# Optimization experiments

Measured on AMD Instinct MI355X. Metric: run time of the kernel, lower is better.

The kernel has to match this reference:

```python
import jax, jax.numpy as jnp
import numpy as np
from jax import lax

NUM_CLASSES = 9
N_BOXES = 6
LEVELS = [(32, 256), (16, 128), (8, 64), (4, 32), (2, 16), (1, 8)]
BATCH = 8


def _conv(x, w, b):
    # x: [N,C,H,W], w: [O,I,3,3] -> same-padded stride-1 conv (padding=1)
    y = lax.conv_general_dilated(x, w, window_strides=(1, 1), padding='SAME',
                                 dimension_numbers=('NCHW', 'OIHW', 'NCHW'))
    return y + b[None, :, None, None]


def _head(x, ws, bs, w_out, b_out):
    for i in range(4):
        x = jax.nn.relu(_conv(x, ws[i], bs[i]))
    return _conv(x, w_out, b_out)


def setup_inputs() -> dict:
    key = jax.random.key(0)
    ks = jax.random.split(key, 12)
    inp = {}
    for i, (h, w) in enumerate(LEVELS):
        inp[f'feat{i}'] = jax.random.normal(ks[i], (BATCH, 256, h, w), dtype=jnp.float32)
    std = 0.01  # matches _init_improved_weights: normal(0, 0.01), bias=0
    inp['reg_w'] = jax.random.normal(ks[6], (4, 256, 256, 3, 3), dtype=jnp.float32) * std
    inp['reg_b'] = jnp.zeros((4, 256), dtype=jnp.float32)
    inp['reg_w_out'] = jax.random.normal(ks[7], (N_BOXES * 4, 256, 3, 3), dtype=jnp.float32) * std
    inp['reg_b_out'] = jnp.zeros((N_BOXES * 4,), dtype=jnp.float32)
    inp['cls_w'] = jax.random.normal(ks[8], (4, 256, 256, 3, 3), dtype=jnp.float32) * std
    inp['cls_b'] = jnp.zeros((4, 256), dtype=jnp.float32)
    inp['cls_w_out'] = jax.random.normal(ks[9], (N_BOXES * NUM_CLASSES, 256, 3, 3), dtype=jnp.float32) * std
    inp['cls_b_out'] = jnp.zeros((N_BOXES * NUM_CLASSES,), dtype=jnp.float32)
    return inp


def reference(feat0, feat1, feat2, feat3, feat4, feat5,
              reg_w, reg_b, reg_w_out, reg_b_out,
              cls_w, cls_b, cls_w_out, cls_b_out):
    features = [feat0, feat1, feat2, feat3, feat4, feat5]
    locations, confidences = [], []
    for x in features:
        n = x.shape[0]
        bbox_delta = _head(x, reg_w, reg_b, reg_w_out, reg_b_out).reshape(n, 4, -1)
        bbox_conf = _head(x, cls_w, cls_b, cls_w_out, cls_b_out).reshape(n, NUM_CLASSES, -1)
        locations.append(bbox_delta)
        confidences.append(bbox_conf)
    bbox_delta = jnp.concatenate(locations, axis=2)   # [N, 4, total_anchors]
    confs = jnp.concatenate(confidences, axis=2)      # [N, num_classes, total_anchors]
    return (bbox_delta, confs)
```

## Files before the change

### kernel.cpp

```cpp
#include <hip/hip_runtime.h>
#include <hip/hip_bf16.h>


typedef float  f32x4 __attribute__((ext_vector_type(4)));
typedef int    i32x4 __attribute__((ext_vector_type(4)));
typedef __bf16 bfrag __attribute__((ext_vector_type(8)));
typedef __bf16 bf4   __attribute__((ext_vector_type(4)));

struct LevelD {
  int H, W, logW, logHW, P, HW, act_off, aoff, blk_start, pos_start;
};
struct Desc  { LevelD lv[6]; };
struct FPtrs { const float* f[6]; };

#define ACT_ELEMS  24735744
#define WREG_OFF   0
#define WCLS_OFF   2359296
#define WREGO_OFF  4718592
#define WCLSO_OFF  4773888
#define ACT0_OFF   4898304
#define ACT1_OFF   29634048
#define WS_ELEMS   54369792ull
#define TOTAL_ANCH 65520
#define CLS_BASE   2096640

__device__ __forceinline__ void glds16(const __bf16* g, __bf16* l) {
  __builtin_amdgcn_global_load_lds(
      (const __attribute__((address_space(1))) void*)g,
      (__attribute__((address_space(3))) void*)l, 16, 0, 0);
}

__device__ __forceinline__ int xcd_swz(int b, int nwg) {
  int xcd = b & 7;
  int q = nwg >> 3, r = nwg & 7;
  int base = (xcd < r) ? xcd * (q + 1) : r * (q + 1) + (xcd - r) * q;
  return base + (b >> 3);
}

__global__ __launch_bounds__(256) void prep_k(const float* __restrict__ w,
                                              __bf16* __restrict__ o, int total)
{
  for (int i = blockIdx.x * 256 + threadIdx.x; i < total; i += gridDim.x * 256) {
    int co = i / 2304;
    int r  = i - co * 2304;
    int t  = r >> 8;
    int ci = r & 255;
    o[i] = (__bf16)w[((co << 8) + ci) * 9 + t];
  }
}

__global__ __launch_bounds__(256) void convert_k(FPtrs fp, __bf16* __restrict__ act, Desc d)
{
  __shared__ __bf16 T[16 * 264];
  int b  = blockIdx.x;
  int p0 = b << 4;
  int li = 0;
  #pragma unroll
  for (int i = 1; i < 6; ++i) li = (p0 >= d.lv[i].pos_start) ? i : li;
  LevelD L = d.lv[li];
  int lp  = b * 16 - L.pos_start;
  int tid = threadIdx.x;
  int pl = tid & 15;
  int p  = lp + pl;
  int n  = p >> L.logHW;
  int y  = (p >> L.logW) & (L.H - 1);
  int x  = p & (L.W - 1);
  const float* src = fp.f[li];
  size_t base = (size_t)n * ((size_t)L.HW << 8) + (size_t)y * L.W + x;
  int c0 = tid >> 4;
  #pragma unroll
  for (int it = 0; it < 16; ++it) {
    int c = c0 + (it << 4);
    T[pl * 264 + c] = (__bf16)src[base + (size_t)c * L.HW];
  }
  __syncthreads();
  int p2 = tid >> 4;
  int cc = (tid & 15) << 4;
  int pg = lp + p2;
  int n2 = pg >> L.logHW;
  int y2 = (pg >> L.logW) & (L.H - 1);
  int x2 = pg & (L.W - 1);
  __bf16* dst = act + L.act_off +
      ((size_t)((n2 * (L.H + 2) + y2 + 1) * (L.W + 2) + x2 + 1) << 8) + cc;
  i32x4 v0 = *(const i32x4*)&T[p2 * 264 + cc];
  i32x4 v1 = *(const i32x4*)&T[p2 * 264 + cc + 8];
  *(i32x4*)dst       = v0;
  *(i32x4*)(dst + 8) = v1;
}

__global__ __launch_bounds__(256, 3)
void conv_mid_k(const __bf16* __restrict__ inb, __bf16* __restrict__ outb,
                const __bf16* __restrict__ wT, const float* __restrict__ bias,
                Desc d)
{
  __shared__ __bf16 Al[2][128 * 32];
  __shared__ __bf16 Bl[2][128 * 32];
  int b  = xcd_swz(blockIdx.x, 1366);
  int li = 0;
  #pragma unroll
  for (int i = 1; i < 6; ++i) li = (b >= d.lv[i].blk_start) ? i : li;
  LevelD L  = d.lv[li];
  int local = b - L.blk_start;
  int mt = local & 1;
  int nt = local >> 1;
  int m0 = mt << 7;
  int p0 = nt << 7;
  int tid  = threadIdx.x;
  int lane = tid & 63;
  int wv   = tid >> 6;
  int wm = wv >> 1, wn = wv & 1;
  int fr = lane & 15, fg = lane >> 4;
  int Wp = L.W + 2;

  int rsub = lane >> 2;
  int slot = lane & 3;
  int sw   = slot ^ ((rsub >> 1) & 3);

  const __bf16* gA[2];
  const __bf16* gB[2];
  int ldsA[2];
  #pragma unroll
  for (int r = 0; r < 2; ++r) {
    int row = (r << 6) + (wv << 4) + rsub;
    gA[r] = wT + (m0 + row) * 2304 + (sw << 3);
    int p  = p0 + row;
    int pc = (p < L.P) ? p : 0;
    int n  = pc >> L.logHW;
    int y  = (pc >> L.logW) & (L.H - 1);
    int x  = pc & (L.W - 1);
    gB[r] = inb + L.act_off + (((n * (L.H + 2) + y) * Wp + x) << 8) + (sw << 3);
    ldsA[r] = ((r << 6) + (wv << 4)) << 5;
  }

  int csw = ((fg ^ ((fr >> 1) & 3)) << 3);
  int offA[4], offB[4];
  #pragma unroll
  for (int f = 0; f < 4; ++f) {
    offA[f] = (((wm << 6) + (f << 4) + fr) << 5) + csw;
    offB[f] = (((wn << 6) + (f << 4) + fr) << 5) + csw;
  }

  auto stage = [&](int k, int bb) {
    int t  = k >> 3;
    int c0 = (k & 7) << 5;
    int ky = (t >= 6) ? 2 : (t >= 3 ? 1 : 0);
    int kx = t - ky * 3;
    int koffA = (t << 8) + c0;
    int koffB = ((ky * Wp + kx) << 8) + c0;
    glds16(gA[0] + koffA, &Al[bb][ldsA[0]]);
    glds16(gA[1] + koffA, &Al[bb][ldsA[1]]);
    glds16(gB[0] + koffB, &Bl[bb][ldsA[0]]);
    glds16(gB[1] + koffB, &Bl[bb][ldsA[1]]);
  };

  f32x4 acc[4][4] = {};

  stage(0, 0);
  #pragma unroll 1
  for (int k = 0; k < 72; ++k) {
    int cur = k & 1;
    __syncthreads();
    if (k < 71) stage(k + 1, cur ^ 1);
    bfrag af[4], bfv[4];
    #pragma unroll
    for (int mf = 0; mf < 4; ++mf) af[mf]  = *(const bfrag*)&Al[cur][offA[mf]];
    #pragma unroll
    for (int nf = 0; nf < 4; ++nf) bfv[nf] = *(const bfrag*)&Bl[cur][offB[nf]];
    #pragma unroll
    for (int mf = 0; mf < 4; ++mf)
      #pragma unroll
      for (int nf = 0; nf < 4; ++nf)
        acc[mf][nf] = __builtin_amdgcn_mfma_f32_16x16x32_bf16(af[mf], bfv[nf],
                                                              acc[mf][nf], 0, 0, 0);
  }

  #pragma unroll
  for (int nf = 0; nf < 4; ++nf) {
    int pp = p0 + (wn << 6) + (nf << 4) + fr;
    if (pp >= L.P) continue;
    int n2 = pp >> L.logHW;
    int y2 = (pp >> L.logW) & (L.H - 1);
    int x2 = pp & (L.W - 1);
    __bf16* ob = outb + L.act_off + (((n2 * (L.H + 2) + y2 + 1) * Wp + x2 + 1) << 8);
    #pragma unroll
    for (int mf = 0; mf < 4; ++mf) {
      int cob = m0 + (wm << 6) + (mf << 4) + (fg << 2);
      f32x4 bb = *(const f32x4*)(bias + cob);
      f32x4 v  = acc[mf][nf];
      bf4 ov;
      #pragma unroll
      for (int j = 0; j < 4; ++j) ov[j] = (__bf16)fmaxf(v[j] + bb[j], 0.0f);
      *(bf4*)(ob + cob) = ov;
    }
  }
}

__global__ __launch_bounds__(256, 3)
void conv_out_k(const __bf16* __restrict__ inb, const __bf16* __restrict__ wT,
                const float* __restrict__ biasO, float* __restrict__ dout,
                Desc d, int Cout, int isCls)
{
  __shared__ __bf16 Asm[2][64 * 32];
  __shared__ __bf16 Bsm[2][128 * 32];
  int b  = xcd_swz(blockIdx.x, 683);
  int li = 0;
  #pragma unroll
  for (int i = 1; i < 6; ++i) li = (b >= d.lv[i].blk_start) ? i : li;
  LevelD L = d.lv[li];
  int p0 = (b - L.blk_start) << 7;
  int tid  = threadIdx.x;
  int lane = tid & 63;
  int wv   = tid >> 6;
  int fr = lane & 15, fg = lane >> 4;
  int Wp = L.W + 2;
  int nmf = (Cout + 15) >> 4;

  int rsub = lane >> 2;
  int slot = lane & 3;
  int sw   = slot ^ ((rsub >> 1) & 3);

  const __bf16* gA0;
  {
    int row = (wv << 4) + rsub;
    int co  = (row < Cout) ? row : 0;
    gA0 = wT + co * 2304 + (sw << 3);
  }
  const __bf16* gB[2];
  #pragma unroll
  for (int j = 0; j < 2; ++j) {
    int row = (j << 6) + (wv << 4) + rsub;
    int p  = p0 + row;
    int pc = (p < L.P) ? p : 0;
    int n = pc >> L.logHW, y = (pc >> L.logW) & (L.H - 1), x = pc & (L.W - 1);
    gB[j] = inb + L.act_off + (((n * (L.H + 2) + y) * Wp + x) << 8) + (sw << 3);
  }
  int dW = (wv << 4) << 5;

  int csw = ((fg ^ ((fr >> 1) & 3)) << 3);
  int offA[4], offB[2];
  #pragma unroll
  for (int mf = 0; mf < 4; ++mf)
    offA[mf] = (((mf << 4) + fr) << 5) + csw;
  #pragma unroll
  for (int nf = 0; nf < 2; ++nf)
    offB[nf] = (((wv << 5) + (nf << 4) + fr) << 5) + csw;

  auto stage = [&](int k, int bb) {
    int t  = k >> 3;
    int ky = (t >= 6) ? 2 : (t >= 3 ? 1 : 0);
    int kx = t - ky * 3;
    int ka = k << 5;
    int kb = ((ky * Wp + kx) << 8) + ((k & 7) << 5);
    glds16(gA0 + ka, &Asm[bb][dW]);
    glds16(gB[0] + kb, &Bsm[bb][dW]);
    glds16(gB[1] + kb, &Bsm[bb][2048 + dW]);
  };

  f32x4 acc[4][2] = {};

  stage(0, 0);
  #pragma unroll 1
  for (int k = 0; k < 72; ++k) {
    int cur = k & 1;
    __syncthreads();
    if (k < 71) stage(k + 1, cur ^ 1);
    bfrag af[4], bfv[2];
    #pragma unroll
    for (int mf = 0; mf < 4; ++mf)
      if (mf < nmf) af[mf] = *(const bfrag*)&Asm[cur][offA[mf]];
    #pragma unroll
    for (int nf = 0; nf < 2; ++nf)
      bfv[nf] = *(const bfrag*)&Bsm[cur][offB[nf]];
    #pragma unroll
    for (int mf = 0; mf < 4; ++mf)
      if (mf < nmf)
        #pragma unroll
        for (int nf = 0; nf < 2; ++nf)
          acc[mf][nf] = __builtin_amdgcn_mfma_f32_16x16x32_bf16(
              af[mf], bfv[nf], acc[mf][nf], 0, 0, 0);
  }

  #pragma unroll
  for (int nf = 0; nf < 2; ++nf) {
    int pp = p0 + (wv << 5) + (nf << 4) + fr;
    if (pp >= L.P) continue;
    int n2 = pp >> L.logHW;
    int y2 = (pp >> L.logW) & (L.H - 1);
    int x2 = pp & (L.W - 1);
    int sp_off = L.aoff + y2 * L.W + x2;
    #pragma unroll
    for (int mf = 0; mf < 4; ++mf) {
      if (mf < nmf) {
        #pragma unroll
        for (int j = 0; j < 4; ++j) {
          int co = (mf << 4) + (fg << 2) + j;
          if (co < Cout) {
            float val = acc[mf][nf][j] + biasO[co];
            int g   = co / 6;
            int box = co - g * 6;
            size_t idx;
            if (isCls) idx = (size_t)CLS_BASE + ((size_t)n2 * 9 + g) * TOTAL_ANCH
                             + sp_off + box * L.HW;
            else       idx = ((size_t)n2 * 4 + g) * TOTAL_ANCH + sp_off + box * L.HW;
            dout[idx] = val;
          }
        }
      }
    }
  }
}

extern "C" void kernel_launch(void* const* d_in, const int* in_sizes, int n_in,
                              void* d_out, int out_size, void* d_ws, size_t ws_size,
                              hipStream_t stream) {
  if (ws_size < WS_ELEMS * 2) return;

  static const int kH[6]      = {32, 16, 8, 4, 2, 1};
  static const int kW[6]      = {256, 128, 64, 32, 16, 8};
  static const int kLogW[6]   = {8, 7, 6, 5, 4, 3};
  static const int kLogHW[6]  = {13, 11, 9, 7, 5, 3};
  static const int kActOff[6] = {0, 17965056, 22757376, 24109056, 24526848, 24674304};
  static const int kAoff[6]   = {0, 49152, 61440, 64512, 65280, 65472};
  static const int kBlkMid[6] = {0, 1024, 1280, 1344, 1360, 1364};
  static const int kBlkOut[6] = {0, 512, 640, 672, 680, 682};
  static const int kPosSt[6]  = {0, 65536, 81920, 86016, 87040, 87296};

  FPtrs fp;
  for (int i = 0; i < 6; ++i) fp.f[i] = (const float*)d_in[i];
  const float* reg_w  = (const float*)d_in[6];
  const float* reg_b  = (const float*)d_in[7];
  const float* reg_wo = (const float*)d_in[8];
  const float* reg_bo = (const float*)d_in[9];
  const float* cls_w  = (const float*)d_in[10];
  const float* cls_b  = (const float*)d_in[11];
  const float* cls_wo = (const float*)d_in[12];
  const float* cls_bo = (const float*)d_in[13];
  __bf16* ws = (__bf16*)d_ws;

  Desc dmid, dout_d;
  for (int i = 0; i < 6; ++i) {
    LevelD L;
    L.H = kH[i]; L.W = kW[i]; L.logW = kLogW[i]; L.logHW = kLogHW[i];
    L.HW = kH[i] * kW[i]; L.P = 8 * L.HW;
    L.act_off = kActOff[i]; L.aoff = kAoff[i];
    L.pos_start = kPosSt[i];
    L.blk_start = kBlkMid[i];
    dmid.lv[i] = L;
    L.blk_start = kBlkOut[i];
    dout_d.lv[i] = L;
  }

  hipMemsetAsync((char*)d_ws + (size_t)ACT0_OFF * 2, 0,
                 (size_t)ACT_ELEMS * 2 * 2, stream);

  prep_k<<<256, 256, 0, stream>>>(reg_w,  ws + WREG_OFF,  1024 * 2304);
  prep_k<<<256, 256, 0, stream>>>(cls_w,  ws + WCLS_OFF,  1024 * 2304);
  prep_k<<<64,  256, 0, stream>>>(reg_wo, ws + WREGO_OFF, 24 * 2304);
  prep_k<<<64,  256, 0, stream>>>(cls_wo, ws + WCLSO_OFF, 54 * 2304);

  for (int head = 0; head < 2; ++head) {
    convert_k<<<5460, 256, 0, stream>>>(fp, ws + ACT0_OFF, dmid);
    const __bf16* wT = ws + (head ? WCLS_OFF : WREG_OFF);
    const float*  bb = head ? cls_b : reg_b;
    conv_mid_k<<<1366, 256, 0, stream>>>(ws + ACT0_OFF, ws + ACT1_OFF, wT + 0 * 589824, bb + 0,   dmid);
    conv_mid_k<<<1366, 256, 0, stream>>>(ws + ACT1_OFF, ws + ACT0_OFF, wT + 1 * 589824, bb + 256, dmid);
    conv_mid_k<<<1366, 256, 0, stream>>>(ws + ACT0_OFF, ws + ACT1_OFF, wT + 2 * 589824, bb + 512, dmid);
    conv_mid_k<<<1366, 256, 0, stream>>>(ws + ACT1_OFF, ws + ACT0_OFF, wT + 3 * 589824, bb + 768, dmid);
    conv_out_k<<<683, 256, 0, stream>>>(ws + ACT0_OFF,
        ws + (head ? WCLSO_OFF : WREGO_OFF), head ? cls_bo : reg_bo,
        (float*)d_out, dout_d, head ? 54 : 24, head);
  }
}
```

Measured before the change: 1.317 ms.

## Restructure mid conv into 8-wave 256x128 tile with triple-buffered staged pipeline

Replaces the 128x128, 4-wave, double-buffered implicit-GEMM conv kernel with a 512-thread kernel. Each block computes all 256 output channels for 128 positions, staging K=64 chunks through a 3-deep LDS ring. Global-to-LDS loads are interleaved between MFMA groups using explicit vmcnt waits, barriers, sched_barrier and setprio. This halves the grid, so each activation tile is loaded once instead of twice, and it aims to hide load latency behind matrix ops. The cost is one block per CU, larger LDS use, and more barriers per iteration.

```diff
diff --git a/kernel.cpp b/kernel.cpp
--- a/kernel.cpp
+++ b/kernel.cpp
@@ -88,23 +88,19 @@
   *(i32x4*)(dst + 8) = v1;
 }
 
-__global__ __launch_bounds__(256, 3)
-void conv_mid_k(const __bf16* __restrict__ inb, __bf16* __restrict__ outb,
-                const __bf16* __restrict__ wT, const float* __restrict__ bias,
-                Desc d)
+__global__ __launch_bounds__(512, 1)
+void conv_mid8_k(const __bf16* __restrict__ inb, __bf16* __restrict__ outb,
+                 const __bf16* __restrict__ wT, const float* __restrict__ bias,
+                 Desc d)
 {
-  __shared__ __bf16 Al[2][128 * 32];
-  __shared__ __bf16 Bl[2][128 * 32];
-  int b  = xcd_swz(blockIdx.x, 1366);
+  __shared__ __bf16 Asm[3 * 16384];
+  __shared__ __bf16 Bsm[3 * 8192];
+  int b  = xcd_swz(blockIdx.x, 683);
   int li = 0;
   #pragma unroll
   for (int i = 1; i < 6; ++i) li = (b >= d.lv[i].blk_start) ? i : li;
-  LevelD L  = d.lv[li];
-  int local = b - L.blk_start;
-  int mt = local & 1;
-  int nt = local >> 1;
-  int m0 = mt << 7;
-  int p0 = nt << 7;
+  LevelD L = d.lv[li];
+  int p0 = (b - L.blk_start) << 7;
   int tid  = threadIdx.x;
   int lane = tid & 63;
   int wv   = tid >> 6;
@@ -112,66 +108,135 @@
   int fr = lane & 15, fg = lane >> 4;
   int Wp = L.W + 2;
 
-  int rsub = lane >> 2;
-  int slot = lane & 3;
-  int sw   = slot ^ ((rsub >> 1) & 3);
-
-  const __bf16* gA[2];
+  int lrow8 = lane >> 3;
+  int lslot = lane & 7;
+  int wvb   = wv << 9;
+
+  const __bf16* gA[4];
+  #pragma unroll
+  for (int r = 0; r < 4; ++r) {
+    int row = (r << 6) + (wv << 3) + lrow8;
+    gA[r] = wT + row * 2304 + ((lslot ^ (row & 7)) << 3);
+  }
   const __bf16* gB[2];
-  int ldsA[2];
   #pragma unroll
   for (int r = 0; r < 2; ++r) {
-    int row = (r << 6) + (wv << 4) + rsub;
-    gA[r] = wT + (m0 + row) * 2304 + (sw << 3);
+    int row = (r << 6) + (wv << 3) + lrow8;
     int p  = p0 + row;
     int pc = (p < L.P) ? p : 0;
-    int n  = pc >> L.logHW;
-    int y  = (pc >> L.logW) & (L.H - 1);
-    int x  = pc & (L.W - 1);
-    gB[r] = inb + L.act_off + (((n * (L.H + 2) + y) * Wp + x) << 8) + (sw << 3);
-    ldsA[r] = ((r << 6) + (wv << 4)) << 5;
-  }
-
-  int csw = ((fg ^ ((fr >> 1) & 3)) << 3);
-  int offA[4], offB[4];
-  #pragma unroll
-  for (int f = 0; f < 4; ++f) {
-    offA[f] = (((wm << 6) + (f << 4) + fr) << 5) + csw;
-    offB[f] = (((wn << 6) + (f << 4) + fr) << 5) + csw;
-  }
-
-  auto stage = [&](int k, int bb) {
-    int t  = k >> 3;
-    int c0 = (k & 7) << 5;
-    int ky = (t >= 6) ? 2 : (t >= 3 ? 1 : 0);
-    int kx = t - ky * 3;
-    int koffA = (t << 8) + c0;
-    int koffB = ((ky * Wp + kx) << 8) + c0;
-    glds16(gA[0] + koffA, &Al[bb][ldsA[0]]);
-    glds16(gA[1] + koffA, &Al[bb][ldsA[1]]);
-    glds16(gB[0] + koffB, &Bl[bb][ldsA[0]]);
-    glds16(gB[1] + koffB, &Bl[bb][ldsA[1]]);
+    int n = pc >> L.logHW, y = (pc >> L.logW) & (L.H - 1), x = pc & (L.W - 1);
+    gB[r] = inb + L.act_off + (((n * (L.H + 2) + y) * Wp + x) << 8)
+            + ((lslot ^ (row & 7)) << 3);
+  }
+
+  int offA[4][2], offB[4][2];
+  #pragma unroll
+  for (int mf = 0; mf < 4; ++mf) {
+    int row = (wm << 6) + (mf << 4) + fr;
+    #pragma unroll
+    for (int kk = 0; kk < 2; ++kk)
+      offA[mf][kk] = (row << 6) + ((((kk << 2) | fg) ^ (row & 7)) << 3);
+  }
+  #pragma unroll
+  for (int nf = 0; nf < 4; ++nf) {
+    int row = (wn << 6) + (nf << 4) + fr;
+    #pragma unroll
+    for (int kk = 0; kk < 2; ++kk)
+      offB[nf][kk] = (row << 6) + ((((kk << 2) | fg) ^ (row & 7)) << 3);
+  }
+
+  auto stageA2 = [&](int k2, int buf, int r0) {
+    int ka = k2 << 6;
+    __bf16* dst = Asm + buf * 16384 + (r0 << 12) + wvb;
+    glds16(gA[r0] + ka, dst);
+    glds16(gA[r0 + 1] + ka, dst + 4096);
   };
+  auto stageB1 = [&](int k2, int buf, int r) {
+    int t2 = k2 >> 2;
+    int ky = (t2 >= 6) ? 2 : (t2 >= 3 ? 1 : 0);
+    int kx = t2 - ky * 3;
+    int kb = ((ky * Wp + kx) << 8) + ((k2 & 3) << 6);
+    glds16(gB[r] + kb, Bsm + buf * 8192 + (r << 12) + wvb);
+  };
 
   f32x4 acc[4][4] = {};
 
-  stage(0, 0);
+  stageA2(0, 0, 0); stageA2(0, 0, 2); stageB1(0, 0, 0); stageB1(0, 0, 1);
+  stageA2(1, 1, 0); stageA2(1, 1, 2); stageB1(1, 1, 0); stageB1(1, 1, 1);
+
+  int cur = 0;
   #pragma unroll 1
-  for (int k = 0; k < 72; ++k) {
-    int cur = k & 1;
-    __syncthreads();
-    if (k < 71) stage(k + 1, cur ^ 1);
-    bfrag af[4], bfv[4];
-    #pragma unroll
-    for (int mf = 0; mf < 4; ++mf) af[mf]  = *(const bfrag*)&Al[cur][offA[mf]];
-    #pragma unroll
-    for (int nf = 0; nf < 4; ++nf) bfv[nf] = *(const bfrag*)&Bl[cur][offB[nf]];
-    #pragma unroll
-    for (int mf = 0; mf < 4; ++mf)
-      #pragma unroll
-      for (int nf = 0; nf < 4; ++nf)
-        acc[mf][nf] = __builtin_amdgcn_mfma_f32_16x16x32_bf16(af[mf], bfv[nf],
-                                                              acc[mf][nf], 0, 0, 0);
+  for (int kt = 0; kt < 36; ++kt) {
+    int s2c = cur + 2; if (s2c >= 3) s2c -= 3;
+    int k2  = kt + 2;
+    bool st = (kt < 34);
+    const __bf16* Ab = Asm + cur * 16384;
+    const __bf16* Bb = Bsm + cur * 8192;
+
+    if (kt == 35) { asm volatile("s_waitcnt vmcnt(0)" ::: "memory"); }
+    else          { asm volatile("s_waitcnt vmcnt(6)" ::: "memory"); }
+    __builtin_amdgcn_s_barrier();
+    asm volatile("" ::: "memory");
+
+    bfrag bfv[4], af0, af1;
+    #pragma unroll
+    for (int nf = 0; nf < 4; ++nf) bfv[nf] = *(const bfrag*)&Bb[offB[nf][0]];
+    af0 = *(const bfrag*)&Ab[offA[0][0]];
+    af1 = *(const bfrag*)&Ab[offA[1][0]];
+    if (st) stageA2(k2, s2c, 0);
+    __builtin_amdgcn_s_barrier();
+    asm volatile("s_waitcnt lgkmcnt(0)" ::: "memory");
+    __builtin_amdgcn_sched_barrier(0);
+    __builtin_amdgcn_s_setprio(1);
+    #pragma unroll
+    for (int nf = 0; nf < 4; ++nf) {
+      acc[0][nf] = __builtin_amdgcn_mfma_f32_16x16x32_bf16(af0, bfv[nf], acc[0][nf], 0, 0, 0);
+      acc[1][nf] = __builtin_amdgcn_mfma_f32_16x16x32_bf16(af1, bfv[nf], acc[1][nf], 0, 0, 0);
+    }
+    __builtin_amdgcn_s_setprio(0);
+    af0 = *(const bfrag*)&Ab[offA[2][0]];
+    af1 = *(const bfrag*)&Ab[offA[3][0]];
+    if (st) stageA2(k2, s2c, 2);
+    __builtin_amdgcn_s_barrier();
+    asm volatile("s_waitcnt lgkmcnt(0)" ::: "memory");
+    __builtin_amdgcn_sched_barrier(0);
+    __builtin_amdgcn_s_setprio(1);
+    #pragma unroll
+    for (int nf = 0; nf < 4; ++nf) {
+      acc[2][nf] = __builtin_amdgcn_mfma_f32_16x16x32_bf16(af0, bfv[nf], acc[2][nf], 0, 0, 0);
+      acc[3][nf] = __builtin_amdgcn_mfma_f32_16x16x32_bf16(af1, bfv[nf], acc[3][nf], 0, 0, 0);
+    }
+    __builtin_amdgcn_s_setprio(0);
+    #pragma unroll
+    for (int nf = 0; nf < 4; ++nf) bfv[nf] = *(const bfrag*)&Bb[offB[nf][1]];
+    af0 = *(const bfrag*)&Ab[offA[0][1]];
+    af1 = *(const bfrag*)&Ab[offA[1][1]];
+    if (st) stageB1(k2, s2c, 0);
+    __builtin_amdgcn_s_barrier();
+    asm volatile("s_waitcnt lgkmcnt(0)" ::: "memory");
+    __builtin_amdgcn_sched_barrier(0);
+    __builtin_amdgcn_s_setprio(1);
+    #pragma unroll
+    for (int nf = 0; nf < 4; ++nf) {
+      acc[0][nf] = __builtin_amdgcn_mfma_f32_16x16x32_bf16(af0, bfv[nf], acc[0][nf], 0, 0, 0);
+      acc[1][nf] = __builtin_amdgcn_mfma_f32_16x16x32_bf16(af1, bfv[nf], acc[1][nf], 0, 0, 0);
+    }
+    __builtin_amdgcn_s_setprio(0);
+    af0 = *(const bfrag*)&Ab[offA[2][1]];
+    af1 = *(const bfrag*)&Ab[offA[3][1]];
+    if (st) stageB1(k2, s2c, 1);
+    __builtin_amdgcn_s_barrier();
+    asm volatile("s_waitcnt lgkmcnt(0)" ::: "memory");
+    __builtin_amdgcn_sched_barrier(0);
+    __builtin_amdgcn_s_setprio(1);
+    #pragma unroll
+    for (int nf = 0; nf < 4; ++nf) {
+      acc[2][nf] = __builtin_amdgcn_mfma_f32_16x16x32_bf16(af0, bfv[nf], acc[2][nf], 0, 0, 0);
+      acc[3][nf] = __builtin_amdgcn_mfma_f32_16x16x32_bf16(af1, bfv[nf], acc[3][nf], 0, 0, 0);
+    }
+    __builtin_amdgcn_s_setprio(0);
+
+    ++cur; if (cur == 3) cur = 0;
   }
 
   #pragma unroll
@@ -184,7 +249,7 @@
     __bf16* ob = outb + L.act_off + (((n2 * (L.H + 2) + y2 + 1) * Wp + x2 + 1) << 8);
     #pragma unroll
     for (int mf = 0; mf < 4; ++mf) {
-      int cob = m0 + (wm << 6) + (mf << 4) + (fg << 2);
+      int cob = (wm << 6) + (mf << 4) + (fg << 2);
       f32x4 bb = *(const f32x4*)(bias + cob);
       f32x4 v  = acc[mf][nf];
       bf4 ov;
@@ -321,8 +386,7 @@
   static const int kLogHW[6]  = {13, 11, 9, 7, 5, 3};
   static const int kActOff[6] = {0, 17965056, 22757376, 24109056, 24526848, 24674304};
   static const int kAoff[6]   = {0, 49152, 61440, 64512, 65280, 65472};
-  static const int kBlkMid[6] = {0, 1024, 1280, 1344, 1360, 1364};
-  static const int kBlkOut[6] = {0, 512, 640, 672, 680, 682};
+  static const int kBlk[6]    = {0, 512, 640, 672, 680, 682};
   static const int kPosSt[6]  = {0, 65536, 81920, 86016, 87040, 87296};
 
   FPtrs fp;
@@ -337,17 +401,14 @@
   const float* cls_bo = (const float*)d_in[13];
   __bf16* ws = (__bf16*)d_ws;
 
-  Desc dmid, dout_d;
+  Desc dd;
   for (int i = 0; i < 6; ++i) {
     LevelD L;
     L.H = kH[i]; L.W = kW[i]; L.logW = kLogW[i]; L.logHW = kLogHW[i];
     L.HW = kH[i] * kW[i]; L.P = 8 * L.HW;
     L.act_off = kActOff[i]; L.aoff = kAoff[i];
-    L.pos_start = kPosSt[i];
-    L.blk_start = kBlkMid[i];
-    dmid.lv[i] = L;
-    L.blk_start = kBlkOut[i];
-    dout_d.lv[i] = L;
+    L.blk_start = kBlk[i]; L.pos_start = kPosSt[i];
+    dd.lv[i] = L;
   }
 
   hipMemsetAsync((char*)d_ws + (size_t)ACT0_OFF * 2, 0,
@@ -359,15 +420,15 @@
   prep_k<<<64,  256, 0, stream>>>(cls_wo, ws + WCLSO_OFF, 54 * 2304);
 
   for (int head = 0; head < 2; ++head) {
-    convert_k<<<5460, 256, 0, stream>>>(fp, ws + ACT0_OFF, dmid);
+    convert_k<<<5460, 256, 0, stream>>>(fp, ws + ACT0_OFF, dd);
     const __bf16* wT = ws + (head ? WCLS_OFF : WREG_OFF);
     const float*  bb = head ? cls_b : reg_b;
-    conv_mid_k<<<1366, 256, 0, stream>>>(ws + ACT0_OFF, ws + ACT1_OFF, wT + 0 * 589824, bb + 0,   dmid);
-    conv_mid_k<<<1366, 256, 0, stream>>>(ws + ACT1_OFF, ws + ACT0_OFF, wT + 1 * 589824, bb + 256, dmid);
-    conv_mid_k<<<1366, 256, 0, stream>>>(ws + ACT0_OFF, ws + ACT1_OFF, wT + 2 * 589824, bb + 512, dmid);
-    conv_mid_k<<<1366, 256, 0, stream>>>(ws + ACT1_OFF, ws + ACT0_OFF, wT + 3 * 589824, bb + 768, dmid);
+    conv_mid8_k<<<683, 512, 0, stream>>>(ws + ACT0_OFF, ws + ACT1_OFF, wT + 0 * 589824, bb + 0,   dd);
+    conv_mid8_k<<<683, 512, 0, stream>>>(ws + ACT1_OFF, ws + ACT0_OFF, wT + 1 * 589824, bb + 256, dd);
+    conv_mid8_k<<<683, 512, 0, stream>>>(ws + ACT0_OFF, ws + ACT1_OFF, wT + 2 * 589824, bb + 512, dd);
+    conv_mid8_k<<<683, 512, 0, stream>>>(ws + ACT1_OFF, ws + ACT0_OFF, wT + 3 * 589824, bb + 768, dd);
     conv_out_k<<<683, 256, 0, stream>>>(ws + ACT0_OFF,
         ws + (head ? WCLSO_OFF : WREGO_OFF), head ? cls_bo : reg_bo,
-        (float*)d_out, dout_d, head ? 54 : 24, head);
-  }
-}
+        (float*)d_out, dd, head ? 54 : 24, head);
+  }
+}
```

New measurement: 1.479 ms. +12.3%, slower.

## Enlarge mid-conv tile to 256x256 with 512 threads and K=64 stages

Applied to the files above, without the earlier changes.

Replaces the 128x128-tile mid conv kernel with a 256 (all output channels) by 256 positions tile per block, using 8 waves, K-step 64 with an XOR-swizzled LDS layout, and s_setprio around MFMA bursts. This halves the loop trips and sync count and removes redundant activation reloads across the two channel tiles. In exchange it uses 128 KB of LDS and 128 accumulator registers per lane, so only one block fits per CU, and the grid drops to 342 blocks, which may leave CUs underfilled.

```diff
diff --git a/kernel.cpp b/kernel.cpp
--- a/kernel.cpp
+++ b/kernel.cpp
@@ -88,90 +88,117 @@
   *(i32x4*)(dst + 8) = v1;
 }
 
-__global__ __launch_bounds__(256, 3)
-void conv_mid_k(const __bf16* __restrict__ inb, __bf16* __restrict__ outb,
-                const __bf16* __restrict__ wT, const float* __restrict__ bias,
-                Desc d)
+__global__ __launch_bounds__(512, 1)
+void conv_mid8_k(const __bf16* __restrict__ inb, __bf16* __restrict__ outb,
+                 const __bf16* __restrict__ wT, const float* __restrict__ bias,
+                 Desc d)
 {
-  __shared__ __bf16 Al[2][128 * 32];
-  __shared__ __bf16 Bl[2][128 * 32];
-  int b  = xcd_swz(blockIdx.x, 1366);
+  __shared__ __bf16 Asm[2][16384];
+  __shared__ __bf16 Bsm[2][16384];
+  int b  = xcd_swz(blockIdx.x, 342);
   int li = 0;
   #pragma unroll
   for (int i = 1; i < 6; ++i) li = (b >= d.lv[i].blk_start) ? i : li;
-  LevelD L  = d.lv[li];
-  int local = b - L.blk_start;
-  int mt = local & 1;
-  int nt = local >> 1;
-  int m0 = mt << 7;
-  int p0 = nt << 7;
+  LevelD L = d.lv[li];
+  int p0 = (b - L.blk_start) << 8;
   int tid  = threadIdx.x;
   int lane = tid & 63;
   int wv   = tid >> 6;
-  int wm = wv >> 1, wn = wv & 1;
+  int wm = wv >> 2, wn = wv & 3;
   int fr = lane & 15, fg = lane >> 4;
   int Wp = L.W + 2;
 
-  int rsub = lane >> 2;
-  int slot = lane & 3;
-  int sw   = slot ^ ((rsub >> 1) & 3);
-
-  const __bf16* gA[2];
-  const __bf16* gB[2];
-  int ldsA[2];
-  #pragma unroll
-  for (int r = 0; r < 2; ++r) {
-    int row = (r << 6) + (wv << 4) + rsub;
-    gA[r] = wT + (m0 + row) * 2304 + (sw << 3);
+  int lrow = lane >> 3;
+  int slot = lane & 7;
+  int dstW = wv << 9;
+
+  const __bf16* gA[4];
+  const __bf16* gB[4];
+  #pragma unroll
+  for (int r = 0; r < 4; ++r) {
+    int row = (r << 6) + (wv << 3) + lrow;
+    int sw  = ((slot ^ (row & 7)) << 3);
+    gA[r] = wT + row * 2304 + sw;
     int p  = p0 + row;
     int pc = (p < L.P) ? p : 0;
-    int n  = pc >> L.logHW;
-    int y  = (pc >> L.logW) & (L.H - 1);
-    int x  = pc & (L.W - 1);
-    gB[r] = inb + L.act_off + (((n * (L.H + 2) + y) * Wp + x) << 8) + (sw << 3);
-    ldsA[r] = ((r << 6) + (wv << 4)) << 5;
-  }
-
-  int csw = ((fg ^ ((fr >> 1) & 3)) << 3);
-  int offA[4], offB[4];
-  #pragma unroll
-  for (int f = 0; f < 4; ++f) {
-    offA[f] = (((wm << 6) + (f << 4) + fr) << 5) + csw;
-    offB[f] = (((wn << 6) + (f << 4) + fr) << 5) + csw;
-  }
-
-  auto stage = [&](int k, int bb) {
-    int t  = k >> 3;
-    int c0 = (k & 7) << 5;
+    int n = pc >> L.logHW, y = (pc >> L.logW) & (L.H - 1), x = pc & (L.W - 1);
+    gB[r] = inb + L.act_off + (((n * (L.H + 2) + y) * Wp + x) << 8) + sw;
+  }
+
+  int offA[8][2], offB[4][2];
+  #pragma unroll
+  for (int mf = 0; mf < 8; ++mf) {
+    int row = (wm << 7) + (mf << 4) + fr;
+    #pragma unroll
+    for (int kk = 0; kk < 2; ++kk)
+      offA[mf][kk] = (row << 6) + ((((kk << 2) | fg) ^ (row & 7)) << 3);
+  }
+  #pragma unroll
+  for (int nf = 0; nf < 4; ++nf) {
+    int row = (wn << 6) + (nf << 4) + fr;
+    #pragma unroll
+    for (int kk = 0; kk < 2; ++kk)
+      offB[nf][kk] = (row << 6) + ((((kk << 2) | fg) ^ (row & 7)) << 3);
+  }
+
+  auto stage = [&](int kt, int buf) {
+    int ka = kt << 6;
+    int t  = kt >> 2;
     int ky = (t >= 6) ? 2 : (t >= 3 ? 1 : 0);
     int kx = t - ky * 3;
-    int koffA = (t << 8) + c0;
-    int koffB = ((ky * Wp + kx) << 8) + c0;
-    glds16(gA[0] + koffA, &Al[bb][ldsA[0]]);
-    glds16(gA[1] + koffA, &Al[bb][ldsA[1]]);
-    glds16(gB[0] + koffB, &Bl[bb][ldsA[0]]);
-    glds16(gB[1] + koffB, &Bl[bb][ldsA[1]]);
+    int kb = ((ky * Wp + kx) << 8) + ((kt & 3) << 6);
+    #pragma unroll
+    for (int r = 0; r < 4; ++r)
+      glds16(gA[r] + ka, &Asm[buf][(r << 12) + dstW]);
+    #pragma unroll
+    for (int r = 0; r < 4; ++r)
+      glds16(gB[r] + kb, &Bsm[buf][(r << 12) + dstW]);
   };
 
-  f32x4 acc[4][4] = {};
+  f32x4 acc[8][4] = {};
+
+  auto compute = [&](int cur) {
+    #pragma unroll
+    for (int mh = 0; mh < 2; ++mh) {
+      bfrag a[4][2];
+      #pragma unroll
+      for (int m = 0; m < 4; ++m)
+        #pragma unroll
+        for (int kk = 0; kk < 2; ++kk)
+          a[m][kk] = *(const bfrag*)&Asm[cur][offA[(mh << 2) + m][kk]];
+      #pragma unroll
+      for (int nh = 0; nh < 2; ++nh) {
+        bfrag bb[2][2];
+        #pragma unroll
+        for (int n2 = 0; n2 < 2; ++n2)
+          #pragma unroll
+          for (int kk = 0; kk < 2; ++kk)
+            bb[n2][kk] = *(const bfrag*)&Bsm[cur][offB[(nh << 1) + n2][kk]];
+        __builtin_amdgcn_s_setprio(1);
+        #pragma unroll
+        for (int m = 0; m < 4; ++m)
+          #pragma unroll
+          for (int n2 = 0; n2 < 2; ++n2)
+            #pragma unroll
+            for (int kk = 0; kk < 2; ++kk)
+              acc[(mh << 2) + m][(nh << 1) + n2] =
+                  __builtin_amdgcn_mfma_f32_16x16x32_bf16(
+                      a[m][kk], bb[n2][kk],
+                      acc[(mh << 2) + m][(nh << 1) + n2], 0, 0, 0);
+        __builtin_amdgcn_s_setprio(0);
+      }
+    }
+  };
 
   stage(0, 0);
+  __syncthreads();
   #pragma unroll 1
-  for (int k = 0; k < 72; ++k) {
-    int cur = k & 1;
+  for (int kt = 0; kt < 36; ++kt) {
+    int cur = kt & 1;
+    if (kt < 35) stage(kt + 1, cur ^ 1);
+    asm volatile("" ::: "memory");
+    compute(cur);
     __syncthreads();
-    if (k < 71) stage(k + 1, cur ^ 1);
-    bfrag af[4], bfv[4];
-    #pragma unroll
-    for (int mf = 0; mf < 4; ++mf) af[mf]  = *(const bfrag*)&Al[cur][offA[mf]];
-    #pragma unroll
-    for (int nf = 0; nf < 4; ++nf) bfv[nf] = *(const bfrag*)&Bl[cur][offB[nf]];
-    #pragma unroll
-    for (int mf = 0; mf < 4; ++mf)
-      #pragma unroll
-      for (int nf = 0; nf < 4; ++nf)
-        acc[mf][nf] = __builtin_amdgcn_mfma_f32_16x16x32_bf16(af[mf], bfv[nf],
-                                                              acc[mf][nf], 0, 0, 0);
   }
 
   #pragma unroll
@@ -183,13 +210,13 @@
     int x2 = pp & (L.W - 1);
     __bf16* ob = outb + L.act_off + (((n2 * (L.H + 2) + y2 + 1) * Wp + x2 + 1) << 8);
     #pragma unroll
-    for (int mf = 0; mf < 4; ++mf) {
-      int cob = m0 + (wm << 6) + (mf << 4) + (fg << 2);
-      f32x4 bb = *(const f32x4*)(bias + cob);
+    for (int mf = 0; mf < 8; ++mf) {
+      int cob = (wm << 7) + (mf << 4) + (fg << 2);
+      f32x4 bv = *(const f32x4*)(bias + cob);
       f32x4 v  = acc[mf][nf];
       bf4 ov;
       #pragma unroll
-      for (int j = 0; j < 4; ++j) ov[j] = (__bf16)fmaxf(v[j] + bb[j], 0.0f);
+      for (int j = 0; j < 4; ++j) ov[j] = (__bf16)fmaxf(v[j] + bv[j], 0.0f);
       *(bf4*)(ob + cob) = ov;
     }
   }
@@ -321,7 +348,7 @@
   static const int kLogHW[6]  = {13, 11, 9, 7, 5, 3};
   static const int kActOff[6] = {0, 17965056, 22757376, 24109056, 24526848, 24674304};
   static const int kAoff[6]   = {0, 49152, 61440, 64512, 65280, 65472};
-  static const int kBlkMid[6] = {0, 1024, 1280, 1344, 1360, 1364};
+  static const int kBlkMid[6] = {0, 256, 320, 336, 340, 341};
   static const int kBlkOut[6] = {0, 512, 640, 672, 680, 682};
   static const int kPosSt[6]  = {0, 65536, 81920, 86016, 87040, 87296};
 
@@ -362,10 +389,10 @@
     convert_k<<<5460, 256, 0, stream>>>(fp, ws + ACT0_OFF, dmid);
     const __bf16* wT = ws + (head ? WCLS_OFF : WREG_OFF);
     const float*  bb = head ? cls_b : reg_b;
-    conv_mid_k<<<1366, 256, 0, stream>>>(ws + ACT0_OFF, ws + ACT1_OFF, wT + 0 * 589824, bb + 0,   dmid);
-    conv_mid_k<<<1366, 256, 0, stream>>>(ws + ACT1_OFF, ws + ACT0_OFF, wT + 1 * 589824, bb + 256, dmid);
-    conv_mid_k<<<1366, 256, 0, stream>>>(ws + ACT0_OFF, ws + ACT1_OFF, wT + 2 * 589824, bb + 512, dmid);
-    conv_mid_k<<<1366, 256, 0, stream>>>(ws + ACT1_OFF, ws + ACT0_OFF, wT + 3 * 589824, bb + 768, dmid);
+    conv_mid8_k<<<342, 512, 0, stream>>>(ws + ACT0_OFF, ws + ACT1_OFF, wT + 0 * 589824, bb + 0,   dmid);
+    conv_mid8_k<<<342, 512, 0, stream>>>(ws + ACT1_OFF, ws + ACT0_OFF, wT + 1 * 589824, bb + 256, dmid);
+    conv_mid8_k<<<342, 512, 0, stream>>>(ws + ACT0_OFF, ws + ACT1_OFF, wT + 2 * 589824, bb + 512, dmid);
+    conv_mid8_k<<<342, 512, 0, stream>>>(ws + ACT1_OFF, ws + ACT0_OFF, wT + 3 * 589824, bb + 768, dmid);
     conv_out_k<<<683, 256, 0, stream>>>(ws + ACT0_OFF,
         ws + (head ? WCLSO_OFF : WREGO_OFF), head ? cls_bo : reg_bo,
         (float*)d_out, dout_d, head ? 54 : 24, head);
```

After: 1.491 ms. 13.1% more time.

## Retile mid convs to full output channels, zero only halos, convert input once

Applied to the files above, without the earlier changes.

The mid 3x3 conv kernel is retiled so each 512-thread block covers all 256 output channels and 96 positions. Activations are then staged once per block instead of once per half of the output channels, which raises reuse of activation loads but changes the accumulator and LDS footprint and occupancy. The full memset of the padded activation buffers becomes a kernel that zeros only the halo border rows and columns. When the workspace is large enough, a third activation buffer holds the converted input, so it is converted once and shared by both heads. The conv_out A-offset expression is rewritten into an equivalent form.

```diff
diff --git a/kernel.cpp b/kernel.cpp
--- a/kernel.cpp
+++ b/kernel.cpp
@@ -4,6 +4,7 @@
 
 typedef float  f32x4 __attribute__((ext_vector_type(4)));
 typedef int    i32x4 __attribute__((ext_vector_type(4)));
+typedef int    i32x2 __attribute__((ext_vector_type(2)));
 typedef __bf16 bfrag __attribute__((ext_vector_type(8)));
 typedef __bf16 bf4   __attribute__((ext_vector_type(4)));
 
@@ -20,9 +21,11 @@
 #define WCLSO_OFF  4773888
 #define ACT0_OFF   4898304
 #define ACT1_OFF   29634048
+#define ACT2_OFF   54369792
 #define WS_ELEMS   54369792ull
 #define TOTAL_ANCH 65520
 #define CLS_BASE   2096640
+#define NPAD_JOBS  9264
 
 __device__ __forceinline__ void glds16(const __bf16* g, __bf16* l) {
   __builtin_amdgcn_global_load_lds(
@@ -35,6 +38,41 @@
   int q = nwg >> 3, r = nwg & 7;
   int base = (xcd < r) ? xcd * (q + 1) : r * (q + 1) + (xcd - r) * q;
   return base + (b >> 3);
+}
+
+__global__ __launch_bounds__(256) void padzero_k(__bf16* __restrict__ act, int nbuf)
+{
+  static const int kHh[6]   = {32, 16, 8, 4, 2, 1};
+  static const int kWw[6]   = {256, 128, 64, 32, 16, 8};
+  static const int kOff[6]  = {0, 17965056, 22757376, 24109056, 24526848, 24674304};
+  static const int kPer[6]  = {580, 292, 148, 76, 40, 22};
+  static const int kCum[7]  = {0, 4640, 6976, 8160, 8768, 9088, 9264};
+  int job  = blockIdx.x * 4 + (threadIdx.x >> 6);
+  int lane = threadIdx.x & 63;
+  int nb = job / NPAD_JOBS;
+  if (nb >= nbuf) return;
+  int e8 = job - nb * NPAD_JOBS;
+  int li = 0;
+  #pragma unroll
+  for (int i = 1; i < 6; ++i) li = (e8 >= kCum[i]) ? i : li;
+  int r = e8 - kCum[li];
+  int per = kPer[li];
+  int n = r / per;
+  int e = r - n * per;
+  int H = kHh[li], W = kWw[li], Wp = W + 2;
+  int y, x;
+  if (e < 2 * Wp) {
+    y = (e < Wp) ? 0 : (H + 1);
+    x = (e < Wp) ? e : (e - Wp);
+  } else {
+    int e2 = e - 2 * Wp;
+    x = (e2 < H) ? 0 : (W + 1);
+    y = 1 + ((e2 < H) ? e2 : (e2 - H));
+  }
+  size_t base = (size_t)nb * ACT_ELEMS + kOff[li]
+              + ((size_t)((n * (H + 2) + y) * Wp + x) << 8) + (lane << 2);
+  i32x2 z = {0, 0};
+  *(i32x2*)(act + base) = z;
 }
 
 __global__ __launch_bounds__(256) void prep_k(const float* __restrict__ w,
@@ -88,23 +126,19 @@
   *(i32x4*)(dst + 8) = v1;
 }
 
-__global__ __launch_bounds__(256, 3)
+__global__ __launch_bounds__(512, 4)
 void conv_mid_k(const __bf16* __restrict__ inb, __bf16* __restrict__ outb,
                 const __bf16* __restrict__ wT, const float* __restrict__ bias,
                 Desc d)
 {
-  __shared__ __bf16 Al[2][128 * 32];
-  __shared__ __bf16 Bl[2][128 * 32];
-  int b  = xcd_swz(blockIdx.x, 1366);
+  __shared__ __bf16 Al[2][256 * 32];
+  __shared__ __bf16 Bl[2][96 * 32];
+  int b  = xcd_swz(blockIdx.x, 912);
   int li = 0;
   #pragma unroll
   for (int i = 1; i < 6; ++i) li = (b >= d.lv[i].blk_start) ? i : li;
-  LevelD L  = d.lv[li];
-  int local = b - L.blk_start;
-  int mt = local & 1;
-  int nt = local >> 1;
-  int m0 = mt << 7;
-  int p0 = nt << 7;
+  LevelD L = d.lv[li];
+  int p0 = (b - L.blk_start) * 96;
   int tid  = threadIdx.x;
   int lane = tid & 63;
   int wv   = tid >> 6;
@@ -117,28 +151,34 @@
   int sw   = slot ^ ((rsub >> 1) & 3);
 
   const __bf16* gA[2];
-  const __bf16* gB[2];
   int ldsA[2];
   #pragma unroll
   for (int r = 0; r < 2; ++r) {
-    int row = (r << 6) + (wv << 4) + rsub;
-    gA[r] = wT + (m0 + row) * 2304 + (sw << 3);
+    int row = (r << 7) + (wv << 4) + rsub;
+    gA[r] = wT + row * 2304 + (sw << 3);
+    ldsA[r] = ((r << 7) + (wv << 4)) << 5;
+  }
+  const __bf16* gB;
+  int ldsB;
+  {
+    int row = (wv << 4) + rsub;
     int p  = p0 + row;
     int pc = (p < L.P) ? p : 0;
     int n  = pc >> L.logHW;
     int y  = (pc >> L.logW) & (L.H - 1);
     int x  = pc & (L.W - 1);
-    gB[r] = inb + L.act_off + (((n * (L.H + 2) + y) * Wp + x) << 8) + (sw << 3);
-    ldsA[r] = ((r << 6) + (wv << 4)) << 5;
+    gB = inb + L.act_off + (((n * (L.H + 2) + y) * Wp + x) << 8) + (sw << 3);
+    ldsB = (wv << 4) << 5;
   }
 
   int csw = ((fg ^ ((fr >> 1) & 3)) << 3);
-  int offA[4], offB[4];
-  #pragma unroll
-  for (int f = 0; f < 4; ++f) {
-    offA[f] = (((wm << 6) + (f << 4) + fr) << 5) + csw;
-    offB[f] = (((wn << 6) + (f << 4) + fr) << 5) + csw;
-  }
+  int offA[4], offB[3];
+  #pragma unroll
+  for (int mf = 0; mf < 4; ++mf)
+    offA[mf] = (((wm << 6) + (mf << 4) + fr) << 5) + csw;
+  #pragma unroll
+  for (int nf = 0; nf < 3; ++nf)
+    offB[nf] = ((wn * 48 + (nf << 4) + fr) << 5) + csw;
 
   auto stage = [&](int k, int bb) {
     int t  = k >> 3;
@@ -149,11 +189,10 @@
     int koffB = ((ky * Wp + kx) << 8) + c0;
     glds16(gA[0] + koffA, &Al[bb][ldsA[0]]);
     glds16(gA[1] + koffA, &Al[bb][ldsA[1]]);
-    glds16(gB[0] + koffB, &Bl[bb][ldsA[0]]);
-    glds16(gB[1] + koffB, &Bl[bb][ldsA[1]]);
+    if (wv < 6) glds16(gB + koffB, &Bl[bb][ldsB]);
   };
 
-  f32x4 acc[4][4] = {};
+  f32x4 acc[4][3] = {};
 
   stage(0, 0);
   #pragma unroll 1
@@ -161,22 +200,22 @@
     int cur = k & 1;
     __syncthreads();
     if (k < 71) stage(k + 1, cur ^ 1);
-    bfrag af[4], bfv[4];
+    bfrag af[4], bfv[3];
     #pragma unroll
     for (int mf = 0; mf < 4; ++mf) af[mf]  = *(const bfrag*)&Al[cur][offA[mf]];
     #pragma unroll
-    for (int nf = 0; nf < 4; ++nf) bfv[nf] = *(const bfrag*)&Bl[cur][offB[nf]];
+    for (int nf = 0; nf < 3; ++nf) bfv[nf] = *(const bfrag*)&Bl[cur][offB[nf]];
     #pragma unroll
     for (int mf = 0; mf < 4; ++mf)
       #pragma unroll
-      for (int nf = 0; nf < 4; ++nf)
+      for (int nf = 0; nf < 3; ++nf)
         acc[mf][nf] = __builtin_amdgcn_mfma_f32_16x16x32_bf16(af[mf], bfv[nf],
                                                               acc[mf][nf], 0, 0, 0);
   }
 
   #pragma unroll
-  for (int nf = 0; nf < 4; ++nf) {
-    int pp = p0 + (wn << 6) + (nf << 4) + fr;
+  for (int nf = 0; nf < 3; ++nf) {
+    int pp = p0 + wn * 48 + (nf << 4) + fr;
     if (pp >= L.P) continue;
     int n2 = pp >> L.logHW;
     int y2 = (pp >> L.logW) & (L.H - 1);
@@ -184,7 +223,7 @@
     __bf16* ob = outb + L.act_off + (((n2 * (L.H + 2) + y2 + 1) * Wp + x2 + 1) << 8);
     #pragma unroll
     for (int mf = 0; mf < 4; ++mf) {
-      int cob = m0 + (wm << 6) + (mf << 4) + (fg << 2);
+      int cob = (wm << 6) + (mf << 4) + (fg << 2);
       f32x4 bb = *(const f32x4*)(bias + cob);
       f32x4 v  = acc[mf][nf];
       bf4 ov;
@@ -249,7 +288,7 @@
     int t  = k >> 3;
     int ky = (t >= 6) ? 2 : (t >= 3 ? 1 : 0);
     int kx = t - ky * 3;
-    int ka = k << 5;
+    int ka = (t << 8) + ((k & 7) << 5);
     int kb = ((ky * Wp + kx) << 8) + ((k & 7) << 5);
     glds16(gA0 + ka, &Asm[bb][dW]);
     glds16(gB[0] + kb, &Bsm[bb][dW]);
@@ -321,7 +360,7 @@
   static const int kLogHW[6]  = {13, 11, 9, 7, 5, 3};
   static const int kActOff[6] = {0, 17965056, 22757376, 24109056, 24526848, 24674304};
   static const int kAoff[6]   = {0, 49152, 61440, 64512, 65280, 65472};
-  static const int kBlkMid[6] = {0, 1024, 1280, 1344, 1360, 1364};
+  static const int kBlkMid[6] = {0, 683, 854, 897, 908, 911};
   static const int kBlkOut[6] = {0, 512, 640, 672, 680, 682};
   static const int kPosSt[6]  = {0, 65536, 81920, 86016, 87040, 87296};
 
@@ -350,24 +389,41 @@
     dout_d.lv[i] = L;
   }
 
-  hipMemsetAsync((char*)d_ws + (size_t)ACT0_OFF * 2, 0,
-                 (size_t)ACT_ELEMS * 2 * 2, stream);
+  bool use3 = ws_size >= (size_t)(ACT0_OFF + 3ull * ACT_ELEMS) * 2ull;
+  int nbuf = use3 ? 3 : 2;
+
+  padzero_k<<<(NPAD_JOBS * nbuf + 3) / 4, 256, 0, stream>>>(ws + ACT0_OFF, nbuf);
 
   prep_k<<<256, 256, 0, stream>>>(reg_w,  ws + WREG_OFF,  1024 * 2304);
   prep_k<<<256, 256, 0, stream>>>(cls_w,  ws + WCLS_OFF,  1024 * 2304);
   prep_k<<<64,  256, 0, stream>>>(reg_wo, ws + WREGO_OFF, 24 * 2304);
   prep_k<<<64,  256, 0, stream>>>(cls_wo, ws + WCLSO_OFF, 54 * 2304);
 
-  for (int head = 0; head < 2; ++head) {
-    convert_k<<<5460, 256, 0, stream>>>(fp, ws + ACT0_OFF, dmid);
-    const __bf16* wT = ws + (head ? WCLS_OFF : WREG_OFF);
-    const float*  bb = head ? cls_b : reg_b;
-    conv_mid_k<<<1366, 256, 0, stream>>>(ws + ACT0_OFF, ws + ACT1_OFF, wT + 0 * 589824, bb + 0,   dmid);
-    conv_mid_k<<<1366, 256, 0, stream>>>(ws + ACT1_OFF, ws + ACT0_OFF, wT + 1 * 589824, bb + 256, dmid);
-    conv_mid_k<<<1366, 256, 0, stream>>>(ws + ACT0_OFF, ws + ACT1_OFF, wT + 2 * 589824, bb + 512, dmid);
-    conv_mid_k<<<1366, 256, 0, stream>>>(ws + ACT1_OFF, ws + ACT0_OFF, wT + 3 * 589824, bb + 768, dmid);
-    conv_out_k<<<683, 256, 0, stream>>>(ws + ACT0_OFF,
-        ws + (head ? WCLSO_OFF : WREGO_OFF), head ? cls_bo : reg_bo,
-        (float*)d_out, dout_d, head ? 54 : 24, head);
-  }
-}
+  if (use3) {
+    convert_k<<<5460, 256, 0, stream>>>(fp, ws + ACT2_OFF, dmid);
+    for (int head = 0; head < 2; ++head) {
+      const __bf16* wT = ws + (head ? WCLS_OFF : WREG_OFF);
+      const float*  bb = head ? cls_b : reg_b;
+      conv_mid_k<<<912, 512, 0, stream>>>(ws + ACT2_OFF, ws + ACT0_OFF, wT + 0 * 589824, bb + 0,   dmid);
+      conv_mid_k<<<912, 512, 0, stream>>>(ws + ACT0_OFF, ws + ACT1_OFF, wT + 1 * 589824, bb + 256, dmid);
+      conv_mid_k<<<912, 512, 0, stream>>>(ws + ACT1_OFF, ws + ACT0_OFF, wT + 2 * 589824, bb + 512, dmid);
+      conv_mid_k<<<912, 512, 0, stream>>>(ws + ACT0_OFF, ws + ACT1_OFF, wT + 3 * 589824, bb + 768, dmid);
+      conv_out_k<<<683, 256, 0, stream>>>(ws + ACT1_OFF,
+          ws + (head ? WCLSO_OFF : WREGO_OFF), head ? cls_bo : reg_bo,
+          (float*)d_out, dout_d, head ? 54 : 24, head);
+    }
+  } else {
+    for (int head = 0; head < 2; ++head) {
+      convert_k<<<5460, 256, 0, stream>>>(fp, ws + ACT0_OFF, dmid);
+      const __bf16* wT = ws + (head ? WCLS_OFF : WREG_OFF);
+      const float*  bb = head ? cls_b : reg_b;
+      conv_mid_k<<<912, 512, 0, stream>>>(ws + ACT0_OFF, ws + ACT1_OFF, wT + 0 * 589824, bb + 0,   dmid);
+      conv_mid_k<<<912, 512, 0, stream>>>(ws + ACT1_OFF, ws + ACT0_OFF, wT + 1 * 589824, bb + 256, dmid);
+      conv_mid_k<<<912, 512, 0, stream>>>(ws + ACT0_OFF, ws + ACT1_OFF, wT + 2 * 589824, bb + 512, dmid);
+      conv_mid_k<<<912, 512, 0, stream>>>(ws + ACT1_OFF, ws + ACT0_OFF, wT + 3 * 589824, bb + 768, dmid);
+      conv_out_k<<<683, 256, 0, stream>>>(ws + ACT0_OFF,
+          ws + (head ? WCLSO_OFF : WREGO_OFF), head ? cls_bo : reg_bo,
+          (float*)d_out, dout_d, head ? 54 : 24, head);
+    }
+  }
+}
```

Measured after the change: 1.243 ms. 5.7% less time.
